# Kernel tuning notes

Hardware: AMD Instinct MI355X
Metric: run time of the kernel (lower is better)

The kernel has to match this reference:

```python
import jax, jax.numpy as jnp
import numpy as np

NG = 16        # ngroup
BIN = 8        # bin_num
BIAS = 3.5     # (bin_num-1)/2
K = 5          # entropy conv kernel size
NMIX = 3       # GMM mixtures
TABLE = 65536.0
NRES = 5       # residual blocks


def _masks():
    # mask A (first layer): strictly-causal raster mask, excludes center pixel
    mA = np.ones((K, K), np.float32)
    mA[K // 2, K // 2:] = 0.0
    mA[K // 2 + 1:, :] = 0.0
    # mask B (hidden/out layers): includes center pixel
    mB = mA.copy()
    mB[K // 2, K // 2] = 1.0
    return jnp.asarray(mA), jnp.asarray(mB)

MASK_A, MASK_B = _masks()


def _gconv(x, w, b, mask):
    # grouped (per-code-group) masked 5x5 conv, SAME padding
    y = jax.lax.conv_general_dilated(
        x, w * mask, (1, 1), [(2, 2), (2, 2)],
        dimension_numbers=('NCHW', 'OIHW', 'NCHW'),
        feature_group_count=NG)
    return y + b[None, :, None, None]


def setup_inputs() -> dict:
    key = jax.random.key(0)
    ks = jax.random.split(key, 6)
    H = W = 384
    data = jax.random.randint(ks[0], (1, NG, H, W), 0, BIN).astype(jnp.int32)
    w1 = jax.random.normal(ks[1], (NG * 3, 1, K, K), jnp.float32) * 0.1
    b1 = jnp.zeros((NG * 3,), jnp.float32)
    rw = jax.random.normal(ks[2], (NRES, 2, NG * 3, 3, K, K), jnp.float32) * 0.05
    rb = jnp.zeros((NRES, 2, NG * 3), jnp.float32)
    wf = jax.random.normal(ks[3], (NG * 3 * NMIX, 3, K, K), jnp.float32) * 0.05
    bf = jnp.zeros((NG * 3 * NMIX,), jnp.float32)
    return dict(data=data, w1=w1, b1=b1, rw=rw, rb=rb, wf=wf, bf=bf)


def reference(data, w1, b1, rw, rb, wf, bf):
    # DInput2: center the quantized code symbols (bias = (bin_num-1)/2 = 3.5)
    x = data.astype(jnp.float32) - BIAS            # [1, NG, H, W]
    h = jax.nn.relu(_gconv(x, w1, b1, MASK_A))     # [1, NG*3, H, W]
    for i in range(NRES):                          # 5 EntropyResidualBlockDBT
        t = jax.nn.relu(_gconv(h, rw[i, 0], rb[i, 0], MASK_B))
        t = jax.nn.relu(_gconv(t, rw[i, 1], rb[i, 1], MASK_B))
        h = h + t
    p = _gconv(h, wf, bf, MASK_B)                  # [1, NG*9, H, W], no act
    B, _, H, W = p.shape
    p = p.reshape(B, NG, NMIX, 3, H, W)
    logit_w, mean, log_s = p[:, :, :, 0], p[:, :, :, 1], p[:, :, :, 2]
    wmix = jax.nn.softmax(logit_w, axis=2)[:, :, :, None]        # [B,NG,M,1,H,W]
    mean = mean[:, :, :, None]
    scale = (jax.nn.softplus(log_s) + 1e-6)[:, :, :, None]
    # bin edges at b +/- 0.5 centered by BIAS -> edges -4.0 .. 4.0
    edges = (jnp.arange(BIN + 1, dtype=jnp.float32) - (BIAS + 0.5))
    edges = edges[None, None, None, :, None, None]
    inv_sqrt2 = jnp.float32(1.0 / np.sqrt(2.0))
    cdf = jnp.sum(wmix * 0.5 * (1.0 + jax.lax.erf((edges - mean) / scale * inv_sqrt2)), axis=2)  # [B,NG,BIN+1,H,W]
    pmf = cdf[:, :, 1:] - cdf[:, :, :-1]           # [B,NG,BIN,H,W]
    # EntropyBatchGmmTable: scale pmf to 16-bit frequency table for the coder
    return pmf * TABLE
```

## Files before the change

### kernel.cpp

```cpp
#include <hip/hip_runtime.h>
#include <math.h>

#define HH 384
#define WW 384
#define NG 16
#define HW (HH*WW)

#define FTW 64
#define FTH 16

template <int PITCH>
__device__ __forceinline__ void accum13(const float* __restrict__ P,
                                        int ty, int tx0,
                                        float (&a)[3][4],
                                        const float (&Wl)[3][13])
{
#pragma unroll
    for (int r = 0; r < 3; ++r) {
        const float* row = P + (ty + r) * PITCH + tx0;
        float4 u0 = *(const float4*)(row);
        float4 u1 = *(const float4*)(row + 4);
        float v[8] = {u0.x, u0.y, u0.z, u0.w, u1.x, u1.y, u1.z, u1.w};
        const int cmax = (r < 2) ? 5 : 3;
#pragma unroll
        for (int c = 0; c < 5; ++c) {
            if (c >= cmax) break;
#pragma unroll
            for (int oc = 0; oc < 3; ++oc) {
                float w = Wl[oc][r * 5 + c];
#pragma unroll
                for (int p = 0; p < 4; ++p)
                    a[oc][p] += w * v[c + p];
            }
        }
    }
}

__global__ __launch_bounds__(256) void conv1_kernel(
    const int* __restrict__ data, const float* __restrict__ w1,
    const float* __restrict__ b1, float* __restrict__ h)
{
    const int g  = blockIdx.z;
    const int x0 = blockIdx.x * FTW, y0 = blockIdx.y * FTH;
    __shared__ __align__(16) float s_in[FTH + 2][FTW + 8];
    const int tid = threadIdx.y * 16 + threadIdx.x;

    const float* wg = w1 + (size_t)g * 3 * 25;
    const float* bg = b1 + (size_t)g * 3;
    float W[3][12];
#pragma unroll
    for (int oc = 0; oc < 3; ++oc)
#pragma unroll
        for (int t = 0; t < 12; ++t)
            W[oc][t] = wg[oc * 25 + t];
    float B[3] = {bg[0], bg[1], bg[2]};

    const int* plane = data + g * HW;
    for (int i = tid; i < 18 * 18; i += 256) {
        int rr = i / 18, q = i % 18;
        int gy = y0 - 2 + rr, gx0 = x0 - 4 + 4 * q;
        float4 v = make_float4(0.f, 0.f, 0.f, 0.f);
        if (gy >= 0) {
            const int* rowp = plane + gy * WW;
            if (gx0 >= 0 && gx0 + 3 < WW) {
                int4 iv = *(const int4*)(rowp + gx0);
                v = make_float4((float)iv.x - 3.5f, (float)iv.y - 3.5f,
                                (float)iv.z - 3.5f, (float)iv.w - 3.5f);
            } else {
                float t[4];
#pragma unroll
                for (int p = 0; p < 4; ++p) {
                    int gx = gx0 + p;
                    t[p] = (gx >= 0 && gx < WW) ? (float)rowp[gx] - 3.5f : 0.f;
                }
                v = make_float4(t[0], t[1], t[2], t[3]);
            }
        }
        *(float4*)&s_in[rr][4 * q] = v;
    }
    __syncthreads();

    const int xg = threadIdx.x, yy = threadIdx.y;
    float a[3][4];
#pragma unroll
    for (int oc = 0; oc < 3; ++oc)
#pragma unroll
        for (int p = 0; p < 4; ++p) a[oc][p] = B[oc];

#pragma unroll
    for (int r = 0; r < 3; ++r) {
        const float* row = &s_in[yy + r][4 * xg];
        float4 u0 = *(const float4*)(row);
        float4 u1 = *(const float4*)(row + 4);
        float4 u2 = *(const float4*)(row + 8);
        float v[12] = {u0.x, u0.y, u0.z, u0.w, u1.x, u1.y, u1.z, u1.w,
                       u2.x, u2.y, u2.z, u2.w};
        const int cmax = (r < 2) ? 5 : 2;
#pragma unroll
        for (int c = 0; c < 5; ++c) {
            if (c >= cmax) break;
#pragma unroll
            for (int oc = 0; oc < 3; ++oc) {
                float w = W[oc][r * 5 + c];
#pragma unroll
                for (int p = 0; p < 4; ++p)
                    a[oc][p] += w * v[c + p + 2];
            }
        }
    }
    const int gy = y0 + yy;
    float* ob = h + (size_t)g * 3 * HW + (size_t)gy * WW + x0 + 4 * xg;
#pragma unroll
    for (int oc = 0; oc < 3; ++oc) {
        *(float4*)(ob + (size_t)oc * HW) =
            make_float4(fmaxf(a[oc][0], 0.f), fmaxf(a[oc][1], 0.f),
                        fmaxf(a[oc][2], 0.f), fmaxf(a[oc][3], 0.f));
    }
}

__global__ __launch_bounds__(256) void res_block_kernel(
    const float* __restrict__ in, const float* __restrict__ wa,
    const float* __restrict__ ba, const float* __restrict__ wb,
    const float* __restrict__ bb, float* __restrict__ out)
{
    const int g  = blockIdx.z;
    const int x0 = blockIdx.x * FTW, y0 = blockIdx.y * FTH;
    __shared__ __align__(16) float IN[3][FTH + 4][FTW + 8];
    __shared__ __align__(16) float T [3][FTH + 2][FTW + 4];
    const int tid = threadIdx.y * 16 + threadIdx.x;

    const float* wga = wa + (size_t)g * 9 * 25;
    const float* bga = ba + (size_t)g * 3;
    const float* wgb = wb + (size_t)g * 9 * 25;
    const float* bgb = bb + (size_t)g * 3;
    float Ba[3] = {bga[0], bga[1], bga[2]};
    float Bb[3] = {bgb[0], bgb[1], bgb[2]};

    const float* base = in + (size_t)g * 3 * HW;
    for (int i = tid; i < 3 * (FTH + 4) * ((FTW + 8) / 4); i += 256) {
        int ch = i / 360, rem = i % 360, rr = rem / 18, q = rem % 18;
        int gy = y0 - 4 + rr, gx0 = x0 - 4 + 4 * q;
        float4 v = make_float4(0.f, 0.f, 0.f, 0.f);
        if (gy >= 0) {
            const float* rowp = base + (size_t)ch * HW + (size_t)gy * WW;
            if (gx0 >= 0 && gx0 + 3 < WW) {
                v = *(const float4*)(rowp + gx0);
            } else {
                float t[4];
#pragma unroll
                for (int p = 0; p < 4; ++p) {
                    int gx = gx0 + p;
                    t[p] = (gx >= 0 && gx < WW) ? rowp[gx] : 0.f;
                }
                v = make_float4(t[0], t[1], t[2], t[3]);
            }
        }
        *(float4*)&IN[ch][rr][4 * q] = v;
    }
    __syncthreads();

    {
        const int i0 = tid, i1 = tid + 256;
        const bool has1 = (i1 < 306);
        const int ty0 = i0 / 17, tx00 = 4 * (i0 % 17);
        const int ty1 = i1 / 17, tx01 = 4 * (i1 % 17);
        float a0[3][4], a1[3][4];
#pragma unroll
        for (int oc = 0; oc < 3; ++oc)
#pragma unroll
            for (int p = 0; p < 4; ++p) { a0[oc][p] = Ba[oc]; a1[oc][p] = Ba[oc]; }

#pragma unroll
        for (int ic = 0; ic < 3; ++ic) {
            float Wl[3][13];
#pragma unroll
            for (int oc = 0; oc < 3; ++oc)
#pragma unroll
                for (int t = 0; t < 13; ++t)
                    Wl[oc][t] = wga[(oc * 3 + ic) * 25 + t];
            accum13<FTW + 8>(&IN[ic][0][0], ty0, tx00, a0, Wl);
            if (has1)
                accum13<FTW + 8>(&IN[ic][0][0], ty1, tx01, a1, Wl);
        }

        {
            int gty = y0 - 2 + ty0, gtx0 = x0 - 2 + tx00;
#pragma unroll
            for (int oc = 0; oc < 3; ++oc) {
                float r_[4];
#pragma unroll
                for (int p = 0; p < 4; ++p) {
                    int gx = gtx0 + p;
                    bool ok = (gty >= 0) && (gx >= 0) && (gx < WW);
                    r_[p] = ok ? fmaxf(a0[oc][p], 0.f) : 0.f;
                }
                *(float4*)&T[oc][ty0][tx00] = make_float4(r_[0], r_[1], r_[2], r_[3]);
            }
        }
        if (has1) {
            int gty = y0 - 2 + ty1, gtx0 = x0 - 2 + tx01;
#pragma unroll
            for (int oc = 0; oc < 3; ++oc) {
                float r_[4];
#pragma unroll
                for (int p = 0; p < 4; ++p) {
                    int gx = gtx0 + p;
                    bool ok = (gty >= 0) && (gx >= 0) && (gx < WW);
                    r_[p] = ok ? fmaxf(a1[oc][p], 0.f) : 0.f;
                }
                *(float4*)&T[oc][ty1][tx01] = make_float4(r_[0], r_[1], r_[2], r_[3]);
            }
        }
    }
    __syncthreads();

    const int xg = threadIdx.x, yy = threadIdx.y;
    float a[3][4];
#pragma unroll
    for (int oc = 0; oc < 3; ++oc)
#pragma unroll
        for (int p = 0; p < 4; ++p) a[oc][p] = Bb[oc];

#pragma unroll
    for (int ic = 0; ic < 3; ++ic) {
        float Wl[3][13];
#pragma unroll
        for (int oc = 0; oc < 3; ++oc)
#pragma unroll
            for (int t = 0; t < 13; ++t)
                Wl[oc][t] = wgb[(oc * 3 + ic) * 25 + t];
        accum13<FTW + 4>(&T[ic][0][0], yy, 4 * xg, a, Wl);
    }

    const int gy = y0 + yy;
    float* ob = out + (size_t)g * 3 * HW + (size_t)gy * WW + x0 + 4 * xg;
#pragma unroll
    for (int oc = 0; oc < 3; ++oc) {
        float4 h0 = *(const float4*)&IN[oc][yy + 4][4 * xg + 4];
        *(float4*)(ob + (size_t)oc * HW) =
            make_float4(h0.x + fmaxf(a[oc][0], 0.f), h0.y + fmaxf(a[oc][1], 0.f),
                        h0.z + fmaxf(a[oc][2], 0.f), h0.w + fmaxf(a[oc][3], 0.f));
    }
}

__device__ __forceinline__ float fast_rcp(float x) {
    return __builtin_amdgcn_rcpf(x);
}

__device__ __forceinline__ float fast_erf(float x) {
    const float a = 0.147f;
    const float c = 1.27323954f;
    float x2 = x * x;
    float ax2 = a * x2;
    float t = x2 * (c + ax2) * fast_rcp(1.f + ax2);
    float e = __expf(-t);
    float s = __builtin_amdgcn_sqrtf(fmaxf(1.f - e, 0.f));
    return copysignf(s, x);
}

__device__ __forceinline__ float fast_softplus(float x) {
    float t = __expf(-fabsf(x));
    return fmaxf(x, 0.f) + __logf(1.f + t);
}

__global__ __launch_bounds__(256) void final_kernel(
    const float* __restrict__ hbuf, const float* __restrict__ wf,
    const float* __restrict__ bf, float* __restrict__ out)
{
    const int g  = blockIdx.z;
    const int x0 = blockIdx.x * FTW, y0 = blockIdx.y * FTH;
    __shared__ __align__(16) float IN[3][FTH + 2][FTW + 8];
    const int tid = threadIdx.y * 16 + threadIdx.x;

    const float* wg = wf + (size_t)g * 9 * 3 * 25;
    const float* bg = bf + (size_t)g * 9;

    const float* base = hbuf + (size_t)g * 3 * HW;
    for (int i = tid; i < 3 * (FTH + 2) * ((FTW + 8) / 4); i += 256) {
        int ch = i / 324, rem = i % 324, rr = rem / 18, q = rem % 18;
        int gy = y0 - 2 + rr, gx0 = x0 - 4 + 4 * q;
        float4 v = make_float4(0.f, 0.f, 0.f, 0.f);
        if (gy >= 0) {
            const float* rowp = base + (size_t)ch * HW + (size_t)gy * WW;
            if (gx0 >= 0 && gx0 + 3 < WW) {
                v = *(const float4*)(rowp + gx0);
            } else {
                float t[4];
#pragma unroll
                for (int p = 0; p < 4; ++p) {
                    int gx = gx0 + p;
                    t[p] = (gx >= 0 && gx < WW) ? rowp[gx] : 0.f;
                }
                v = make_float4(t[0], t[1], t[2], t[3]);
            }
        }
        *(float4*)&IN[ch][rr][4 * q] = v;
    }
    __syncthreads();

    const int xg = threadIdx.x, yy = threadIdx.y;
    float P[9][4];
#pragma unroll
    for (int m = 0; m < 9; ++m) {
        float b = bg[m];
#pragma unroll
        for (int p = 0; p < 4; ++p) P[m][p] = b;
    }

#pragma unroll
    for (int ic = 0; ic < 3; ++ic) {
        float v[3][12];
#pragma unroll
        for (int r = 0; r < 3; ++r) {
            const float* row = &IN[ic][yy + r][4 * xg];
            float4 u0 = *(const float4*)(row);
            float4 u1 = *(const float4*)(row + 4);
            float4 u2 = *(const float4*)(row + 8);
            v[r][0] = u0.x; v[r][1] = u0.y; v[r][2]  = u0.z; v[r][3]  = u0.w;
            v[r][4] = u1.x; v[r][5] = u1.y; v[r][6]  = u1.z; v[r][7]  = u1.w;
            v[r][8] = u2.x; v[r][9] = u2.y; v[r][10] = u2.z; v[r][11] = u2.w;
        }
#pragma unroll
        for (int m = 0; m < 9; ++m) {
            float Wm[13];
#pragma unroll
            for (int t = 0; t < 13; ++t)
                Wm[t] = wg[(m * 3 + ic) * 25 + t];
#pragma unroll
            for (int r = 0; r < 3; ++r) {
                const int cmax = (r < 2) ? 5 : 3;
#pragma unroll
                for (int c = 0; c < 5; ++c) {
                    if (c >= cmax) break;
                    float w = Wm[r * 5 + c];
#pragma unroll
                    for (int p = 0; p < 4; ++p)
                        P[m][p] += w * v[r][c + p + 2];
                }
            }
        }
    }

    const float inv_sqrt2 = 0.70710678118654752440f;
    float wm0[4], wm1[4], wm2[4], mu0[4], mu1[4], mu2[4], k0[4], k1[4], k2[4];
#pragma unroll
    for (int p = 0; p < 4; ++p) {
        float lw0 = P[0][p], m0 = P[1][p], ls0 = P[2][p];
        float lw1 = P[3][p], m1 = P[4][p], ls1 = P[5][p];
        float lw2 = P[6][p], m2 = P[7][p], ls2 = P[8][p];
        float lmax = fmaxf(lw0, fmaxf(lw1, lw2));
        float e0 = __expf(lw0 - lmax), e1 = __expf(lw1 - lmax), e2 = __expf(lw2 - lmax);
        float inv_sum = fast_rcp(e0 + e1 + e2);
        wm0[p] = 0.5f * e0 * inv_sum;
        wm1[p] = 0.5f * e1 * inv_sum;
        wm2[p] = 0.5f * e2 * inv_sum;
        mu0[p] = m0; mu1[p] = m1; mu2[p] = m2;
        k0[p] = inv_sqrt2 * fast_rcp(fast_softplus(ls0) + 1e-6f);
        k1[p] = inv_sqrt2 * fast_rcp(fast_softplus(ls1) + 1e-6f);
        k2[p] = inv_sqrt2 * fast_rcp(fast_softplus(ls2) + 1e-6f);
    }

    const int gy = y0 + yy;
    float* ob = out + ((size_t)g * 8 * HH + gy) * WW + x0 + 4 * xg;
    float prev[4] = {0.f, 0.f, 0.f, 0.f};
#pragma unroll
    for (int j = 0; j <= 8; ++j) {
        float edge = (float)j - 4.0f;
        float cdf[4];
#pragma unroll
        for (int p = 0; p < 4; ++p) {
            cdf[p] = wm0[p] * (1.f + fast_erf((edge - mu0[p]) * k0[p]))
                   + wm1[p] * (1.f + fast_erf((edge - mu1[p]) * k1[p]))
                   + wm2[p] * (1.f + fast_erf((edge - mu2[p]) * k2[p]));
        }
        if (j > 0) {
            *(float4*)(ob + (size_t)(j - 1) * HW) =
                make_float4((cdf[0] - prev[0]) * 65536.f, (cdf[1] - prev[1]) * 65536.f,
                            (cdf[2] - prev[2]) * 65536.f, (cdf[3] - prev[3]) * 65536.f);
        }
#pragma unroll
        for (int p = 0; p < 4; ++p) prev[p] = cdf[p];
    }
}

extern "C" void kernel_launch(void* const* d_in, const int* in_sizes, int n_in,
                              void* d_out, int out_size, void* d_ws, size_t ws_size,
                              hipStream_t stream)
{
    const int*   data = (const int*)d_in[0];
    const float* w1   = (const float*)d_in[1];
    const float* b1   = (const float*)d_in[2];
    const float* rw   = (const float*)d_in[3];
    const float* rb   = (const float*)d_in[4];
    const float* wf   = (const float*)d_in[5];
    const float* bf   = (const float*)d_in[6];
    float* out = (float*)d_out;

    float* A = (float*)d_ws;
    float* B = A + (size_t)48 * HW;

    dim3 blk(16, 16, 1);
    dim3 grd(WW / FTW, HH / FTH, NG);

    conv1_kernel<<<grd, blk, 0, stream>>>(data, w1, b1, A);

    const float* cur = A;
    float* nxt = B;
    for (int i = 0; i < 5; ++i) {
        const float* wa = rw + (size_t)(i * 2 + 0) * 48 * 3 * 25;
        const float* ba = rb + (i * 2 + 0) * 48;
        const float* wb = rw + (size_t)(i * 2 + 1) * 48 * 3 * 25;
        const float* bb = rb + (i * 2 + 1) * 48;
        res_block_kernel<<<grd, blk, 0, stream>>>(cur, wa, ba, wb, bb, nxt);
        const float* t = cur; cur = nxt; nxt = (float*)t;
    }
    final_kernel<<<grd, blk, 0, stream>>>(cur, wf, bf, out);
}
```

Measured before the change: 334.0 us.

## Use logistic normal-CDF approximation, interior fast-path loads, and scalar weight reads

Replaces the erf-based CDF with a logistic-polynomial approximation of the normal CDF that needs one exp and one reciprocal per mixture. Mean and scale are folded into one FMA. Interior tiles in the residual and final kernels load halos with unguarded float4 reads. Weights are read directly from uniform memory instead of being staged in register arrays, and the two-tile first stage of the residual block becomes a rolled loop. These changes aim to cut transcendental and register cost at a small accuracy risk.

```diff
diff --git a/kernel.cpp b/kernel.cpp
--- a/kernel.cpp
+++ b/kernel.cpp
@@ -47,13 +47,6 @@
 
     const float* wg = w1 + (size_t)g * 3 * 25;
     const float* bg = b1 + (size_t)g * 3;
-    float W[3][12];
-#pragma unroll
-    for (int oc = 0; oc < 3; ++oc)
-#pragma unroll
-        for (int t = 0; t < 12; ++t)
-            W[oc][t] = wg[oc * 25 + t];
-    float B[3] = {bg[0], bg[1], bg[2]};
 
     const int* plane = data + g * HW;
     for (int i = tid; i < 18 * 18; i += 256) {
@@ -85,7 +78,7 @@
 #pragma unroll
     for (int oc = 0; oc < 3; ++oc)
 #pragma unroll
-        for (int p = 0; p < 4; ++p) a[oc][p] = B[oc];
+        for (int p = 0; p < 4; ++p) a[oc][p] = bg[oc];
 
 #pragma unroll
     for (int r = 0; r < 3; ++r) {
@@ -101,7 +94,7 @@
             if (c >= cmax) break;
 #pragma unroll
             for (int oc = 0; oc < 3; ++oc) {
-                float w = W[oc][r * 5 + c];
+                float w = wg[oc * 25 + r * 5 + c];
 #pragma unroll
                 for (int p = 0; p < 4; ++p)
                     a[oc][p] += w * v[c + p + 2];
@@ -133,58 +126,63 @@
     const float* bga = ba + (size_t)g * 3;
     const float* wgb = wb + (size_t)g * 9 * 25;
     const float* bgb = bb + (size_t)g * 3;
-    float Ba[3] = {bga[0], bga[1], bga[2]};
-    float Bb[3] = {bgb[0], bgb[1], bgb[2]};
 
     const float* base = in + (size_t)g * 3 * HW;
-    for (int i = tid; i < 3 * (FTH + 4) * ((FTW + 8) / 4); i += 256) {
-        int ch = i / 360, rem = i % 360, rr = rem / 18, q = rem % 18;
-        int gy = y0 - 4 + rr, gx0 = x0 - 4 + 4 * q;
-        float4 v = make_float4(0.f, 0.f, 0.f, 0.f);
-        if (gy >= 0) {
-            const float* rowp = base + (size_t)ch * HW + (size_t)gy * WW;
-            if (gx0 >= 0 && gx0 + 3 < WW) {
-                v = *(const float4*)(rowp + gx0);
-            } else {
-                float t[4];
-#pragma unroll
-                for (int p = 0; p < 4; ++p) {
-                    int gx = gx0 + p;
-                    t[p] = (gx >= 0 && gx < WW) ? rowp[gx] : 0.f;
+    const bool interior = (y0 >= 4) && (x0 >= 4) && (x0 + 68 <= WW);
+    if (interior) {
+        for (int i = tid; i < 1080; i += 256) {
+            int ch = i / 360, rem = i % 360, rr = rem / 18, q = rem % 18;
+            const float* rowp = base + (size_t)ch * HW
+                              + (size_t)(y0 - 4 + rr) * WW + (x0 - 4 + 4 * q);
+            *(float4*)&IN[ch][rr][4 * q] = *(const float4*)rowp;
+        }
+    } else {
+        for (int i = tid; i < 1080; i += 256) {
+            int ch = i / 360, rem = i % 360, rr = rem / 18, q = rem % 18;
+            int gy = y0 - 4 + rr, gx0 = x0 - 4 + 4 * q;
+            float4 v = make_float4(0.f, 0.f, 0.f, 0.f);
+            if (gy >= 0) {
+                const float* rowp = base + (size_t)ch * HW + (size_t)gy * WW;
+                if (gx0 >= 0 && gx0 + 3 < WW) {
+                    v = *(const float4*)(rowp + gx0);
+                } else {
+                    float t[4];
+#pragma unroll
+                    for (int p = 0; p < 4; ++p) {
+                        int gx = gx0 + p;
+                        t[p] = (gx >= 0 && gx < WW) ? rowp[gx] : 0.f;
+                    }
+                    v = make_float4(t[0], t[1], t[2], t[3]);
                 }
-                v = make_float4(t[0], t[1], t[2], t[3]);
-            }
-        }
-        *(float4*)&IN[ch][rr][4 * q] = v;
+            }
+            *(float4*)&IN[ch][rr][4 * q] = v;
+        }
     }
     __syncthreads();
 
-    {
-        const int i0 = tid, i1 = tid + 256;
-        const bool has1 = (i1 < 306);
-        const int ty0 = i0 / 17, tx00 = 4 * (i0 % 17);
-        const int ty1 = i1 / 17, tx01 = 4 * (i1 % 17);
-        float a0[3][4], a1[3][4];
-#pragma unroll
-        for (int oc = 0; oc < 3; ++oc)
-#pragma unroll
-            for (int p = 0; p < 4; ++p) { a0[oc][p] = Ba[oc]; a1[oc][p] = Ba[oc]; }
-
-#pragma unroll
-        for (int ic = 0; ic < 3; ++ic) {
-            float Wl[3][13];
+#pragma unroll 1
+    for (int it = 0; it < 2; ++it) {
+        const int i = tid + (it << 8);
+        if (i < 306) {
+            const int ty = i / 17, tx0 = 4 * (i % 17);
+            float a[3][4];
 #pragma unroll
             for (int oc = 0; oc < 3; ++oc)
 #pragma unroll
-                for (int t = 0; t < 13; ++t)
-                    Wl[oc][t] = wga[(oc * 3 + ic) * 25 + t];
-            accum13<FTW + 8>(&IN[ic][0][0], ty0, tx00, a0, Wl);
-            if (has1)
-                accum13<FTW + 8>(&IN[ic][0][0], ty1, tx01, a1, Wl);
-        }
-
-        {
-            int gty = y0 - 2 + ty0, gtx0 = x0 - 2 + tx00;
+                for (int p = 0; p < 4; ++p) a[oc][p] = bga[oc];
+
+#pragma unroll
+            for (int ic = 0; ic < 3; ++ic) {
+                float Wl[3][13];
+#pragma unroll
+                for (int oc = 0; oc < 3; ++oc)
+#pragma unroll
+                    for (int t = 0; t < 13; ++t)
+                        Wl[oc][t] = wga[(oc * 3 + ic) * 25 + t];
+                accum13<FTW + 8>(&IN[ic][0][0], ty, tx0, a, Wl);
+            }
+
+            const int gty = y0 - 2 + ty, gtx0 = x0 - 2 + tx0;
 #pragma unroll
             for (int oc = 0; oc < 3; ++oc) {
                 float r_[4];
@@ -192,23 +190,9 @@
                 for (int p = 0; p < 4; ++p) {
                     int gx = gtx0 + p;
                     bool ok = (gty >= 0) && (gx >= 0) && (gx < WW);
-                    r_[p] = ok ? fmaxf(a0[oc][p], 0.f) : 0.f;
+                    r_[p] = ok ? fmaxf(a[oc][p], 0.f) : 0.f;
                 }
-                *(float4*)&T[oc][ty0][tx00] = make_float4(r_[0], r_[1], r_[2], r_[3]);
-            }
-        }
-        if (has1) {
-            int gty = y0 - 2 + ty1, gtx0 = x0 - 2 + tx01;
-#pragma unroll
-            for (int oc = 0; oc < 3; ++oc) {
-                float r_[4];
-#pragma unroll
-                for (int p = 0; p < 4; ++p) {
-                    int gx = gtx0 + p;
-                    bool ok = (gty >= 0) && (gx >= 0) && (gx < WW);
-                    r_[p] = ok ? fmaxf(a1[oc][p], 0.f) : 0.f;
-                }
-                *(float4*)&T[oc][ty1][tx01] = make_float4(r_[0], r_[1], r_[2], r_[3]);
+                *(float4*)&T[oc][ty][tx0] = make_float4(r_[0], r_[1], r_[2], r_[3]);
             }
         }
     }
@@ -219,7 +203,7 @@
 #pragma unroll
     for (int oc = 0; oc < 3; ++oc)
 #pragma unroll
-        for (int p = 0; p < 4; ++p) a[oc][p] = Bb[oc];
+        for (int p = 0; p < 4; ++p) a[oc][p] = bgb[oc];
 
 #pragma unroll
     for (int ic = 0; ic < 3; ++ic) {
@@ -245,17 +229,6 @@
 
 __device__ __forceinline__ float fast_rcp(float x) {
     return __builtin_amdgcn_rcpf(x);
-}
-
-__device__ __forceinline__ float fast_erf(float x) {
-    const float a = 0.147f;
-    const float c = 1.27323954f;
-    float x2 = x * x;
-    float ax2 = a * x2;
-    float t = x2 * (c + ax2) * fast_rcp(1.f + ax2);
-    float e = __expf(-t);
-    float s = __builtin_amdgcn_sqrtf(fmaxf(1.f - e, 0.f));
-    return copysignf(s, x);
 }
 
 __device__ __forceinline__ float fast_softplus(float x) {
@@ -276,25 +249,35 @@
     const float* bg = bf + (size_t)g * 9;
 
     const float* base = hbuf + (size_t)g * 3 * HW;
-    for (int i = tid; i < 3 * (FTH + 2) * ((FTW + 8) / 4); i += 256) {
-        int ch = i / 324, rem = i % 324, rr = rem / 18, q = rem % 18;
-        int gy = y0 - 2 + rr, gx0 = x0 - 4 + 4 * q;
-        float4 v = make_float4(0.f, 0.f, 0.f, 0.f);
-        if (gy >= 0) {
-            const float* rowp = base + (size_t)ch * HW + (size_t)gy * WW;
-            if (gx0 >= 0 && gx0 + 3 < WW) {
-                v = *(const float4*)(rowp + gx0);
-            } else {
-                float t[4];
-#pragma unroll
-                for (int p = 0; p < 4; ++p) {
-                    int gx = gx0 + p;
-                    t[p] = (gx >= 0 && gx < WW) ? rowp[gx] : 0.f;
+    const bool interior = (y0 >= 2) && (x0 >= 4) && (x0 + 68 <= WW);
+    if (interior) {
+        for (int i = tid; i < 972; i += 256) {
+            int ch = i / 324, rem = i % 324, rr = rem / 18, q = rem % 18;
+            const float* rowp = base + (size_t)ch * HW
+                              + (size_t)(y0 - 2 + rr) * WW + (x0 - 4 + 4 * q);
+            *(float4*)&IN[ch][rr][4 * q] = *(const float4*)rowp;
+        }
+    } else {
+        for (int i = tid; i < 972; i += 256) {
+            int ch = i / 324, rem = i % 324, rr = rem / 18, q = rem % 18;
+            int gy = y0 - 2 + rr, gx0 = x0 - 4 + 4 * q;
+            float4 v = make_float4(0.f, 0.f, 0.f, 0.f);
+            if (gy >= 0) {
+                const float* rowp = base + (size_t)ch * HW + (size_t)gy * WW;
+                if (gx0 >= 0 && gx0 + 3 < WW) {
+                    v = *(const float4*)(rowp + gx0);
+                } else {
+                    float t[4];
+#pragma unroll
+                    for (int p = 0; p < 4; ++p) {
+                        int gx = gx0 + p;
+                        t[p] = (gx >= 0 && gx < WW) ? rowp[gx] : 0.f;
+                    }
+                    v = make_float4(t[0], t[1], t[2], t[3]);
                 }
-                v = make_float4(t[0], t[1], t[2], t[3]);
-            }
-        }
-        *(float4*)&IN[ch][rr][4 * q] = v;
+            }
+            *(float4*)&IN[ch][rr][4 * q] = v;
+        }
     }
     __syncthreads();
 
@@ -322,17 +305,13 @@
         }
 #pragma unroll
         for (int m = 0; m < 9; ++m) {
-            float Wm[13];
-#pragma unroll
-            for (int t = 0; t < 13; ++t)
-                Wm[t] = wg[(m * 3 + ic) * 25 + t];
 #pragma unroll
             for (int r = 0; r < 3; ++r) {
                 const int cmax = (r < 2) ? 5 : 3;
 #pragma unroll
                 for (int c = 0; c < 5; ++c) {
                     if (c >= cmax) break;
-                    float w = Wm[r * 5 + c];
+                    float w = wg[(m * 3 + ic) * 25 + r * 5 + c];
 #pragma unroll
                     for (int p = 0; p < 4; ++p)
                         P[m][p] += w * v[r][c + p + 2];
@@ -341,8 +320,7 @@
         }
     }
 
-    const float inv_sqrt2 = 0.70710678118654752440f;
-    float wm0[4], wm1[4], wm2[4], mu0[4], mu1[4], mu2[4], k0[4], k1[4], k2[4];
+    float wm0[4], wm1[4], wm2[4], ks0[4], ks1[4], ks2[4], nm0[4], nm1[4], nm2[4];
 #pragma unroll
     for (int p = 0; p < 4; ++p) {
         float lw0 = P[0][p], m0 = P[1][p], ls0 = P[2][p];
@@ -351,13 +329,15 @@
         float lmax = fmaxf(lw0, fmaxf(lw1, lw2));
         float e0 = __expf(lw0 - lmax), e1 = __expf(lw1 - lmax), e2 = __expf(lw2 - lmax);
         float inv_sum = fast_rcp(e0 + e1 + e2);
-        wm0[p] = 0.5f * e0 * inv_sum;
-        wm1[p] = 0.5f * e1 * inv_sum;
-        wm2[p] = 0.5f * e2 * inv_sum;
-        mu0[p] = m0; mu1[p] = m1; mu2[p] = m2;
-        k0[p] = inv_sqrt2 * fast_rcp(fast_softplus(ls0) + 1e-6f);
-        k1[p] = inv_sqrt2 * fast_rcp(fast_softplus(ls1) + 1e-6f);
-        k2[p] = inv_sqrt2 * fast_rcp(fast_softplus(ls2) + 1e-6f);
+        wm0[p] = e0 * inv_sum;
+        wm1[p] = e1 * inv_sum;
+        wm2[p] = e2 * inv_sum;
+        ks0[p] = fast_rcp(fast_softplus(ls0) + 1e-6f);
+        ks1[p] = fast_rcp(fast_softplus(ls1) + 1e-6f);
+        ks2[p] = fast_rcp(fast_softplus(ls2) + 1e-6f);
+        nm0[p] = -m0 * ks0[p];
+        nm1[p] = -m1 * ks1[p];
+        nm2[p] = -m2 * ks2[p];
     }
 
     const int gy = y0 + yy;
@@ -369,9 +349,16 @@
         float cdf[4];
 #pragma unroll
         for (int p = 0; p < 4; ++p) {
-            cdf[p] = wm0[p] * (1.f + fast_erf((edge - mu0[p]) * k0[p]))
-                   + wm1[p] * (1.f + fast_erf((edge - mu1[p]) * k1[p]))
-                   + wm2[p] * (1.f + fast_erf((edge - mu2[p]) * k2[p]));
+            float z0 = fmaf(edge, ks0[p], nm0[p]);
+            float z1 = fmaf(edge, ks1[p], nm1[p]);
+            float z2 = fmaf(edge, ks2[p], nm2[p]);
+            float y0_ = z0 * fmaf(z0 * z0, -0.07056f, -1.5976f);
+            float y1_ = z1 * fmaf(z1 * z1, -0.07056f, -1.5976f);
+            float y2_ = z2 * fmaf(z2 * z2, -0.07056f, -1.5976f);
+            float c = wm0[p] * fast_rcp(1.f + __expf(y0_));
+            c = fmaf(wm1[p], fast_rcp(1.f + __expf(y1_)), c);
+            c = fmaf(wm2[p], fast_rcp(1.f + __expf(y2_)), c);
+            cdf[p] = c;
         }
         if (j > 0) {
             *(float4*)(ob + (size_t)(j - 1) * HW) =
```

New measurement: 319.2 us. -4.4%, faster.
